# Performance work log

Hardware: AMD Instinct MI355X
Metric: run time of the kernel (lower is better)

The kernel has to match this reference:

```python
import jax, jax.numpy as jnp
import numpy as np

B = 65536
PEP, TCR, D, FF = 384, 480, 128, 512
H1, H2, OUT = 128, 64, 1
EPS = 1e-5


def _ln(x, g, b):
    mu = jnp.mean(x, axis=-1, keepdims=True)
    var = jnp.mean((x - mu) ** 2, axis=-1, keepdims=True)
    return (x - mu) * jax.lax.rsqrt(var + EPS) * g + b


def _bn(x, g, b):
    # training-mode BatchNorm1d: batch-wide stats, biased variance
    mu = jnp.mean(x, axis=0, keepdims=True)
    var = jnp.mean((x - mu) ** 2, axis=0, keepdims=True)
    return (x - mu) * jax.lax.rsqrt(var + EPS) * g + b


def setup_inputs() -> dict:
    key = jax.random.key(0)
    ks = iter(jax.random.split(key, 40))

    def w(shape, fan):
        s = float(np.sqrt(6.0 / fan))
        return jax.random.uniform(next(ks), shape, jnp.float32, -s, s)

    inp = {
        "x": jax.random.normal(next(ks), (B, PEP + TCR), jnp.float32),
        "w_pep": w((D, PEP), PEP + D), "b_pep": jnp.zeros(D),
        "w_tcr": w((D, TCR), TCR + D), "b_tcr": jnp.zeros(D),
        "wv_p2t": w((D, D), 2 * D), "bv_p2t": jnp.zeros(D),
        "wo_p2t": w((D, D), 2 * D), "bo_p2t": jnp.zeros(D),
        "wv_t2p": w((D, D), 2 * D), "bv_t2p": jnp.zeros(D),
        "wo_t2p": w((D, D), 2 * D), "bo_t2p": jnp.zeros(D),
        "ln_g1p": jnp.ones(D), "ln_b1p": jnp.zeros(D),
        "ln_g2p": jnp.ones(D), "ln_b2p": jnp.zeros(D),
        "ln_g1t": jnp.ones(D), "ln_b1t": jnp.zeros(D),
        "ln_g2t": jnp.ones(D), "ln_b2t": jnp.zeros(D),
        "ffn_w1p": w((FF, D), D + FF), "ffn_b1p": jnp.zeros(FF),
        "ffn_w2p": w((D, FF), D + FF), "ffn_b2p": jnp.zeros(D),
        "ffn_w1t": w((FF, D), D + FF), "ffn_b1t": jnp.zeros(FF),
        "ffn_w2t": w((D, FF), D + FF), "ffn_b2t": jnp.zeros(D),
        "w_h1": w((H1, 2 * D), 2 * D + H1), "b_h1": jnp.zeros(H1),
        "bn1_g": jnp.ones(H1), "bn1_b": jnp.zeros(H1),
        "w_h2": w((H2, H1), H1 + H2), "b_h2": jnp.zeros(H2),
        "bn2_g": jnp.ones(H2), "bn2_b": jnp.zeros(H2),
        "w_out": w((OUT, H2), H2 + OUT), "b_out": jnp.zeros(OUT),
    }
    return inp


def reference(x, w_pep, b_pep, w_tcr, b_tcr,
              wv_p2t, bv_p2t, wo_p2t, bo_p2t,
              wv_t2p, bv_t2p, wo_t2p, bo_t2p,
              ln_g1p, ln_b1p, ln_g2p, ln_b2p,
              ln_g1t, ln_b1t, ln_g2t, ln_b2t,
              ffn_w1p, ffn_b1p, ffn_w2p, ffn_b2p,
              ffn_w1t, ffn_b1t, ffn_w2t, ffn_b2t,
              w_h1, b_h1, bn1_g, bn1_b,
              w_h2, b_h2, bn2_g, bn2_b,
              w_out, b_out):
    pep = x[:, :PEP] @ w_pep.T + b_pep   # (B, 128)
    tcr = x[:, PEP:] @ w_tcr.T + b_tcr   # (B, 128)

    # MHA with seq_len=1: softmax over single key == 1 exactly,
    # so attention output = out_proj(v_proj(key/value input)).
    pa = (tcr @ wv_p2t.T + bv_p2t) @ wo_p2t.T + bo_p2t
    pa = _ln(pep + pa, ln_g1p, ln_b1p)
    h = jax.nn.gelu(pa @ ffn_w1p.T + ffn_b1p, approximate=False)
    pa = _ln(pa + h @ ffn_w2p.T + ffn_b2p, ln_g2p, ln_b2p)

    ta = (pep @ wv_t2p.T + bv_t2p) @ wo_t2p.T + bo_t2p
    ta = _ln(tcr + ta, ln_g1t, ln_b1t)
    h = jax.nn.gelu(ta @ ffn_w1t.T + ffn_b1t, approximate=False)
    ta = _ln(ta + h @ ffn_w2t.T + ffn_b2t, ln_g2t, ln_b2t)

    combined = jnp.concatenate([pa, ta], axis=1)  # (B, 256)
    h1 = jax.nn.gelu(_bn(combined @ w_h1.T + b_h1, bn1_g, bn1_b), approximate=False)
    h2 = jax.nn.gelu(_bn(h1 @ w_h2.T + b_h2, bn2_g, bn2_b), approximate=False)
    return h2 @ w_out.T + b_out  # (B, 1)
```

## Files before the change

kernel.cpp:

```cpp
#include <hip/hip_runtime.h>
#include <hip/hip_bf16.h>
#include <math.h>


typedef __attribute__((ext_vector_type(8))) __bf16 bf16x8;
typedef __attribute__((ext_vector_type(8))) short s16x8;
typedef __attribute__((ext_vector_type(4))) float f32x4;

union S8U { s16x8 s; bf16x8 b; };

__device__ __forceinline__ short f2b(float f) {
  return __builtin_bit_cast(short, (__bf16)f);
}
__device__ __forceinline__ float b2f(short s) {
  union { unsigned u; float f; } v; v.u = ((unsigned)(unsigned short)s) << 16;
  return v.f;
}
__device__ __forceinline__ float gelu_f(float x) {
  float u = x * __builtin_fmaf(0.035677408136f, x * x, 0.7978845608028654f);
  float e = __expf(-2.0f * u);
  return x * __builtin_amdgcn_rcpf(1.0f + e);
}

template<int NTS>
__device__ __forceinline__ void mfma_step(const short* __restrict__ Abuf, int lda, int kkA,
                                          const short* __restrict__ W, int ldw, int kw,
                                          int colbase, int l16, int q,
                                          f32x4 (&acc)[4][NTS]) {
  S8U a[4];
#pragma unroll
  for (int mt = 0; mt < 4; ++mt)
    a[mt].s = *(const s16x8*)(Abuf + (16 * mt + l16) * lda + kkA + 8 * q);
#pragma unroll
  for (int nt = 0; nt < NTS; ++nt) {
    S8U b;
    b.s = *(const s16x8*)(W + (size_t)(colbase + 16 * nt + l16) * ldw + kw + 8 * q);
#pragma unroll
    for (int mt = 0; mt < 4; ++mt)
      acc[mt][nt] = __builtin_amdgcn_mfma_f32_16x16x32_bf16(a[mt].b, b.b, acc[mt][nt], 0, 0, 0);
  }
}

template<int NTS>
__device__ __forceinline__ void zero_acc(f32x4 (&acc)[4][NTS]) {
  f32x4 z = {0.f, 0.f, 0.f, 0.f};
#pragma unroll
  for (int mt = 0; mt < 4; ++mt)
#pragma unroll
    for (int nt = 0; nt < NTS; ++nt) acc[mt][nt] = z;
}

__device__ __forceinline__ void epi_bias_store(f32x4 (&acc)[4][2], const float* __restrict__ bias,
                                               short* dst, int w, int l16, int q, bool do_gelu) {
#pragma unroll
  for (int nt = 0; nt < 2; ++nt) {
    int col = 32 * w + 16 * nt + l16;
    float bb = bias[col];
#pragma unroll
    for (int mt = 0; mt < 4; ++mt)
#pragma unroll
      for (int r = 0; r < 4; ++r) {
        int row = 16 * mt + 4 * q + r;
        float v = acc[mt][nt][r] + bb;
        if (do_gelu) v = gelu_f(v);
        dst[row * 136 + col] = f2b(v);
      }
  }
}

__device__ __forceinline__ void epi_res_ln(f32x4 (&acc)[4][2], const float* __restrict__ bias,
                                           const short* resbuf,
                                           const float* __restrict__ g, const float* __restrict__ bta,
                                           short* dst, float (*lnp)[4][2], float (*murs)[2],
                                           int w, int l16, int q, int tid) {
#pragma unroll
  for (int nt = 0; nt < 2; ++nt) {
    int col = 32 * w + 16 * nt + l16;
    float bb = bias[col];
#pragma unroll
    for (int mt = 0; mt < 4; ++mt)
#pragma unroll
      for (int r = 0; r < 4; ++r) {
        int row = 16 * mt + 4 * q + r;
        acc[mt][nt][r] += bb + b2f(resbuf[row * 136 + col]);
      }
  }
#pragma unroll
  for (int mt = 0; mt < 4; ++mt) {
#pragma unroll
    for (int r = 0; r < 4; ++r) {
      float v0 = acc[mt][0][r], v1 = acc[mt][1][r];
      float s = v0 + v1;
      float sq = v0 * v0 + v1 * v1;
#pragma unroll
      for (int off = 1; off < 16; off <<= 1) {
        s += __shfl_xor(s, off);
        sq += __shfl_xor(sq, off);
      }
      if (l16 == 0) {
        int row = 16 * mt + 4 * q + r;
        lnp[row][w][0] = s;
        lnp[row][w][1] = sq;
      }
    }
  }
  __syncthreads();
  if (tid < 64) {
    float s = lnp[tid][0][0] + lnp[tid][1][0] + lnp[tid][2][0] + lnp[tid][3][0];
    float sq = lnp[tid][0][1] + lnp[tid][1][1] + lnp[tid][2][1] + lnp[tid][3][1];
    float mu = s * (1.0f / 128.0f);
    float var = sq * (1.0f / 128.0f) - mu * mu;
    murs[tid][0] = mu;
    murs[tid][1] = rsqrtf(var + 1e-5f);
  }
  __syncthreads();
#pragma unroll
  for (int nt = 0; nt < 2; ++nt) {
    int col = 32 * w + 16 * nt + l16;
    float gg = g[col], b2 = bta[col];
#pragma unroll
    for (int mt = 0; mt < 4; ++mt)
#pragma unroll
      for (int r = 0; r < 4; ++r) {
        int row = 16 * mt + 4 * q + r;
        float v = (acc[mt][nt][r] - murs[row][0]) * murs[row][1] * gg + b2;
        dst[row * 136 + col] = f2b(v);
      }
  }
}

__device__ __forceinline__ void ffn_block(const short* __restrict__ w1, const short* __restrict__ w2,
                                          const float* __restrict__ b1, const float* __restrict__ b2,
                                          const float* __restrict__ g, const float* __restrict__ bta,
                                          short* act, short* H,
                                          float (*lnp)[4][2], float (*murs)[2],
                                          int w, int l16, int q, int tid) {
  f32x4 acc2[4][2];
  zero_acc(acc2);
  for (int c = 0; c < 4; ++c) {
    f32x4 acch[4][2];
    zero_acc(acch);
#pragma unroll
    for (int kk = 0; kk < 4; ++kk)
      mfma_step<2>(act, 136, 32 * kk, w1, 128, 32 * kk, c * 128 + 32 * w, l16, q, acch);
#pragma unroll
    for (int nt = 0; nt < 2; ++nt) {
      int lcol = 32 * w + 16 * nt + l16;
      float bb = b1[c * 128 + lcol];
#pragma unroll
      for (int mt = 0; mt < 4; ++mt)
#pragma unroll
        for (int r = 0; r < 4; ++r)
          H[(16 * mt + 4 * q + r) * 136 + lcol] = f2b(gelu_f(acch[mt][nt][r] + bb));
    }
    __syncthreads();
#pragma unroll
    for (int kk = 0; kk < 4; ++kk)
      mfma_step<2>(H, 136, 32 * kk, w2, 512, c * 128 + 32 * kk, 32 * w, l16, q, acc2);
    __syncthreads();
  }
  epi_res_ln(acc2, b2, act, g, bta, act, lnp, murs, w, l16, q, tid);
  __syncthreads();
}

struct K1Args {
  const float* x;
  const short *wpep, *wtcr, *wcp, *wct, *w1p, *w2p, *w1t, *w2t, *wh1;
  const float *bpep, *btcr, *bcp, *bct;
  const float *g1p, *e1p, *g2p, *e2p, *g1t, *e1t, *g2t, *e2t;
  const float *b1p, *b2p, *b1t, *b2t, *bh1;
  float *sum1, *sq1;
  short* h1;
};

__global__ __launch_bounds__(256, 3) void k1_main(K1Args A) {
  __shared__ __align__(16) short smem[2 * 64 * 136 + 2 * 64 * 72];
  short* U = smem;
  short* V = U + 64 * 136;
  short* Rst = V + 64 * 136;
  short* R0 = Rst;
  short* R1 = Rst + 64 * 72;
  short* Hb = Rst;
  float (*lnp)[4][2] = (float (*)[4][2])(void*)(Rst + 7936);
  float (*murs)[2] = (float (*)[2])(void*)(Rst + 8960);

  const int tid = threadIdx.x;
  const int w = tid >> 6;
  const int lane = tid & 63;
  const int l16 = lane & 15;
  const int q = lane >> 4;
  const size_t row0 = (size_t)blockIdx.x * 64;

  const int r_st = tid >> 2;
  const float* xrow = A.x + (row0 + r_st) * 864;

  float4 pf0, pf1, pf2, pf3;
  auto issue64 = [&](int kb) {
    const float* p = xrow + kb + (tid & 3) * 16;
    pf0 = *(const float4*)(p);
    pf1 = *(const float4*)(p + 4);
    pf2 = *(const float4*)(p + 8);
    pf3 = *(const float4*)(p + 12);
  };
  auto write64 = [&](short* Sb) {
    int c = (tid & 3) * 16;
    s16x8 o0, o1;
    o0[0] = f2b(pf0.x); o0[1] = f2b(pf0.y); o0[2] = f2b(pf0.z); o0[3] = f2b(pf0.w);
    o0[4] = f2b(pf1.x); o0[5] = f2b(pf1.y); o0[6] = f2b(pf1.z); o0[7] = f2b(pf1.w);
    o1[0] = f2b(pf2.x); o1[1] = f2b(pf2.y); o1[2] = f2b(pf2.z); o1[3] = f2b(pf2.w);
    o1[4] = f2b(pf3.x); o1[5] = f2b(pf3.y); o1[6] = f2b(pf3.z); o1[7] = f2b(pf3.w);
    *(s16x8*)(Sb + r_st * 72 + c) = o0;
    *(s16x8*)(Sb + r_st * 72 + c + 8) = o1;
  };
  auto issue32 = [&](int kb) {
    const float* p = xrow + kb + (tid & 3) * 8;
    pf0 = *(const float4*)(p);
    pf1 = *(const float4*)(p + 4);
  };
  auto write32 = [&](short* Sb) {
    int c = (tid & 3) * 8;
    s16x8 o0;
    o0[0] = f2b(pf0.x); o0[1] = f2b(pf0.y); o0[2] = f2b(pf0.z); o0[3] = f2b(pf0.w);
    o0[4] = f2b(pf1.x); o0[5] = f2b(pf1.y); o0[6] = f2b(pf1.z); o0[7] = f2b(pf1.w);
    *(s16x8*)(Sb + r_st * 72 + c) = o0;
  };

  f32x4 accP[4][2], accT[4][2];
  zero_acc(accP); zero_acc(accT);

  issue64(0); write64(R0);
  __syncthreads();
  for (int t = 0; t < 14; ++t) {
    short* cur = (t & 1) ? R1 : R0;
    short* nxt = (t & 1) ? R0 : R1;
    if (t < 13) { if (t == 12) issue32(832); else issue64(64 * (t + 1)); }
    if (t < 6) {
      mfma_step<2>(cur, 72, 0,  A.wpep, 384, 64 * t,      32 * w, l16, q, accP);
      mfma_step<2>(cur, 72, 32, A.wpep, 384, 64 * t + 32, 32 * w, l16, q, accP);
    } else if (t < 13) {
      mfma_step<2>(cur, 72, 0,  A.wtcr, 480, 64 * (t - 6),      32 * w, l16, q, accT);
      mfma_step<2>(cur, 72, 32, A.wtcr, 480, 64 * (t - 6) + 32, 32 * w, l16, q, accT);
    } else {
      mfma_step<2>(cur, 72, 0,  A.wtcr, 480, 448, 32 * w, l16, q, accT);
    }
    if (t < 13) { if (t == 12) write32(nxt); else write64(nxt); }
    __syncthreads();
  }
  epi_bias_store(accP, A.bpep, U, w, l16, q, false);
  epi_bias_store(accT, A.btcr, V, w, l16, q, false);
  __syncthreads();

  zero_acc(accP); zero_acc(accT);
#pragma unroll
  for (int kk = 0; kk < 4; ++kk)
    mfma_step<2>(V, 136, 32 * kk, A.wcp, 128, 32 * kk, 32 * w, l16, q, accP);
#pragma unroll
  for (int kk = 0; kk < 4; ++kk)
    mfma_step<2>(U, 136, 32 * kk, A.wct, 128, 32 * kk, 32 * w, l16, q, accT);
  epi_res_ln(accP, A.bcp, U, A.g1p, A.e1p, U, lnp, murs, w, l16, q, tid);
  epi_res_ln(accT, A.bct, V, A.g1t, A.e1t, V, lnp, murs, w, l16, q, tid);
  __syncthreads();

  ffn_block(A.w1p, A.w2p, A.b1p, A.b2p, A.g2p, A.e2p, U, Hb, lnp, murs, w, l16, q, tid);
  ffn_block(A.w1t, A.w2t, A.b1t, A.b2t, A.g2t, A.e2t, V, Hb, lnp, murs, w, l16, q, tid);

  zero_acc(accP);
#pragma unroll
  for (int s = 0; s < 8; ++s)
    mfma_step<2>((s < 4) ? U : V, 136, 32 * (s & 3), A.wh1, 256, 32 * s, 32 * w, l16, q, accP);
#pragma unroll
  for (int nt = 0; nt < 2; ++nt) {
    int col = 32 * w + 16 * nt + l16;
    float bb = A.bh1[col];
    float s = 0.f, sq = 0.f;
#pragma unroll
    for (int mt = 0; mt < 4; ++mt)
#pragma unroll
      for (int r = 0; r < 4; ++r) {
        float v = accP[mt][nt][r] + bb;
        s += v; sq += v * v;
        A.h1[(row0 + 16 * mt + 4 * q + r) * 128 + col] = f2b(v);
      }
    s += __shfl_xor(s, 16); sq += __shfl_xor(sq, 16);
    s += __shfl_xor(s, 32); sq += __shfl_xor(sq, 32);
    if (q == 0) {
      atomicAdd(&A.sum1[col], s);
      atomicAdd(&A.sq1[col], sq);
    }
  }
}

struct K2Args {
  const short* h1;
  const short* wh2;
  const float *bh2, *bn1g, *bn1b;
  const float *sum1, *sq1;
  float *sum2, *sq2;
  short* h2;
};

__global__ __launch_bounds__(256) void k2_main(K2Args A) {
  __shared__ __align__(16) short S2[64 * 136];
  __shared__ float s1[128], t1[128];
  const int tid = threadIdx.x;
  const int w = tid >> 6, lane = tid & 63, l16 = lane & 15, q = lane >> 4;
  const size_t row0 = (size_t)blockIdx.x * 64;

  if (tid < 128) {
    float su = A.sum1[tid], sq = A.sq1[tid];
    float mu = su * (1.0f / 65536.0f);
    float var = sq * (1.0f / 65536.0f) - mu * mu;
    float sc = A.bn1g[tid] * rsqrtf(var + 1e-5f);
    s1[tid] = sc;
    t1[tid] = A.bn1b[tid] - mu * sc;
  }
  __syncthreads();
  {
    int r = tid >> 2;
#pragma unroll
    for (int j = 0; j < 4; ++j) {
      int c = (tid & 3) * 32 + j * 8;
      s16x8 hv = *(const s16x8*)(A.h1 + (row0 + r) * 128 + c);
      s16x8 o;
#pragma unroll
      for (int i = 0; i < 8; ++i) {
        float f = b2f(hv[i]);
        f = gelu_f(f * s1[c + i] + t1[c + i]);
        o[i] = f2b(f);
      }
      *(s16x8*)(S2 + r * 136 + c) = o;
    }
  }
  __syncthreads();
  f32x4 acc[4][1];
  zero_acc(acc);
#pragma unroll
  for (int kk = 0; kk < 4; ++kk)
    mfma_step<1>(S2, 136, 32 * kk, A.wh2, 128, 32 * kk, 16 * w, l16, q, acc);
  int col = 16 * w + l16;
  float bb = A.bh2[col];
  float s = 0.f, sq = 0.f;
#pragma unroll
  for (int mt = 0; mt < 4; ++mt)
#pragma unroll
    for (int r = 0; r < 4; ++r) {
      float v = acc[mt][0][r] + bb;
      s += v; sq += v * v;
      A.h2[(row0 + 16 * mt + 4 * q + r) * 64 + col] = f2b(v);
    }
  s += __shfl_xor(s, 16); sq += __shfl_xor(sq, 16);
  s += __shfl_xor(s, 32); sq += __shfl_xor(sq, 32);
  if (q == 0) {
    atomicAdd(&A.sum2[col], s);
    atomicAdd(&A.sq2[col], sq);
  }
}

struct K3Args {
  const short* h2;
  const float *bn2g, *bn2b;
  const float *sum2, *sq2;
  const float *wout, *bout;
  float* out;
};

__global__ __launch_bounds__(256) void k3_main(K3Args A) {
  __shared__ float s2[64], t2[64], wo[64];
  const int tid = threadIdx.x;
  if (tid < 64) {
    float su = A.sum2[tid], sq = A.sq2[tid];
    float mu = su * (1.0f / 65536.0f);
    float var = sq * (1.0f / 65536.0f) - mu * mu;
    float sc = A.bn2g[tid] * rsqrtf(var + 1e-5f);
    s2[tid] = sc;
    t2[tid] = A.bn2b[tid] - mu * sc;
    wo[tid] = A.wout[tid];
  }
  __syncthreads();
  size_t row = (size_t)blockIdx.x * 32 + (tid >> 3);
  int c0 = (tid & 7) * 8;
  s16x8 hv = *(const s16x8*)(A.h2 + row * 64 + c0);
  float s = 0.f;
#pragma unroll
  for (int i = 0; i < 8; ++i) {
    float f = b2f(hv[i]);
    f = gelu_f(f * s2[c0 + i] + t2[c0 + i]);
    s += f * wo[c0 + i];
  }
  s += __shfl_xor(s, 1); s += __shfl_xor(s, 2); s += __shfl_xor(s, 4);
  if ((tid & 7) == 0) A.out[row] = s + A.bout[0];
}

struct CvtArgs {
  const float* src[8];
  short* dst;
  float* stats;
  const float *wv[2], *wo[2], *bv[2], *bo[2];
  short* wc[2];
  float* bc[2];
};

__global__ __launch_bounds__(256) void k0_setup(CvtArgs A) {
  int b = blockIdx.x;
  const int tid = threadIdx.x;
  if (b >= 404) {
    int b2 = b - 404, pair = b2 >> 4, part = b2 & 15;
    const float* wv = A.wv[pair];
    const float* wo = A.wo[pair];
#pragma unroll
    for (int i = 0; i < 4; ++i) {
      int idx = part * 1024 + i * 256 + tid;
      int o = idx >> 7, k = idx & 127;
      const float* worow = wo + o * 128;
      float acc = 0.f;
#pragma unroll 4
      for (int j = 0; j < 128; ++j) acc += worow[j] * wv[j * 128 + k];
      A.wc[pair][idx] = f2b(acc);
    }
    if (part == 0 && tid < 128) {
      const float* bvp = A.bv[pair];
      float acc = A.bo[pair][tid];
      for (int j = 0; j < 128; ++j) acc += wo[tid * 128 + j] * bvp[j];
      A.bc[pair][tid] = acc;
    }
    return;
  }
  const int st[8] = {0, 49152, 176128, 241664, 307200, 372736, 438272, 471040};
  if (b == 0) {
    A.stats[tid] = 0.0f;
    if (tid < 128) A.stats[256 + tid] = 0.0f;
  }
  int dstbase = b * 1024 + ((b >= 108) ? 65536 : 0);
  int seg = 0;
#pragma unroll
  for (int t = 1; t < 8; ++t) seg += (dstbase >= st[t]) ? 1 : 0;
  const float* s = A.src[seg];
  int loc = dstbase - st[seg] + tid * 4;
  float4 f = *(const float4*)(s + loc);
  int di = dstbase + tid * 4;
  A.dst[di + 0] = f2b(f.x);
  A.dst[di + 1] = f2b(f.y);
  A.dst[di + 2] = f2b(f.z);
  A.dst[di + 3] = f2b(f.w);
}

extern "C" void kernel_launch(void* const* d_in, const int* in_sizes, int n_in,
                              void* d_out, int out_size, void* d_ws, size_t ws_size,
                              hipStream_t stream) {
  (void)in_sizes; (void)n_in; (void)out_size; (void)ws_size;
  const float* x = (const float*)d_in[0];
  char* ws = (char*)d_ws;
  short* wb = (short*)ws;
  enum { O_PEP = 0, O_TCR = 49152, O_WCP = 110592, O_BCF = 126976,
         O_WCT = 143360, O_W1P = 176128, O_W2P = 241664,
         O_W1T = 307200, O_W2T = 372736, O_H1 = 438272, O_H2 = 471040 };
  float* stats = (float*)(ws + 958464);
  short* h1_pre = (short*)(ws + 960000);
  short* h2_pre = (short*)(ws + 17737216);
  float* bcomp = (float*)(ws + (size_t)O_BCF * 2);

  CvtArgs ca;
  ca.src[0] = (const float*)d_in[1];
  ca.src[1] = (const float*)d_in[3];
  ca.src[2] = (const float*)d_in[21];
  ca.src[3] = (const float*)d_in[23];
  ca.src[4] = (const float*)d_in[25];
  ca.src[5] = (const float*)d_in[27];
  ca.src[6] = (const float*)d_in[29];
  ca.src[7] = (const float*)d_in[33];
  ca.dst = wb;
  ca.stats = stats;
  ca.wv[0] = (const float*)d_in[5];   ca.bv[0] = (const float*)d_in[6];
  ca.wo[0] = (const float*)d_in[7];   ca.bo[0] = (const float*)d_in[8];
  ca.wv[1] = (const float*)d_in[9];   ca.bv[1] = (const float*)d_in[10];
  ca.wo[1] = (const float*)d_in[11];  ca.bo[1] = (const float*)d_in[12];
  ca.wc[0] = wb + O_WCP;  ca.wc[1] = wb + O_WCT;
  ca.bc[0] = bcomp;       ca.bc[1] = bcomp + 128;
  k0_setup<<<436, 256, 0, stream>>>(ca);

  K1Args a1;
  a1.x = x;
  a1.wpep = wb + O_PEP;  a1.wtcr = wb + O_TCR;
  a1.wcp = wb + O_WCP;   a1.wct = wb + O_WCT;
  a1.w1p = wb + O_W1P;   a1.w2p = wb + O_W2P;
  a1.w1t = wb + O_W1T;   a1.w2t = wb + O_W2T;
  a1.wh1 = wb + O_H1;
  a1.bpep = (const float*)d_in[2];
  a1.btcr = (const float*)d_in[4];
  a1.bcp = bcomp;
  a1.bct = bcomp + 128;
  a1.g1p = (const float*)d_in[13];  a1.e1p = (const float*)d_in[14];
  a1.g2p = (const float*)d_in[15];  a1.e2p = (const float*)d_in[16];
  a1.g1t = (const float*)d_in[17];  a1.e1t = (const float*)d_in[18];
  a1.g2t = (const float*)d_in[19];  a1.e2t = (const float*)d_in[20];
  a1.b1p = (const float*)d_in[22];
  a1.b2p = (const float*)d_in[24];
  a1.b1t = (const float*)d_in[26];
  a1.b2t = (const float*)d_in[28];
  a1.bh1 = (const float*)d_in[30];
  a1.sum1 = stats;
  a1.sq1 = stats + 128;
  a1.h1 = h1_pre;
  k1_main<<<1024, 256, 0, stream>>>(a1);

  K2Args a2;
  a2.h1 = h1_pre;
  a2.wh2 = wb + O_H2;
  a2.bh2 = (const float*)d_in[34];
  a2.bn1g = (const float*)d_in[31];
  a2.bn1b = (const float*)d_in[32];
  a2.sum1 = stats;
  a2.sq1 = stats + 128;
  a2.sum2 = stats + 256;
  a2.sq2 = stats + 320;
  a2.h2 = h2_pre;
  k2_main<<<1024, 256, 0, stream>>>(a2);

  K3Args a3;
  a3.h2 = h2_pre;
  a3.bn2g = (const float*)d_in[35];
  a3.bn2b = (const float*)d_in[36];
  a3.sum2 = stats + 256;
  a3.sq2 = stats + 320;
  a3.wout = (const float*)d_in[37];
  a3.bout = (const float*)d_in[38];
  a3.out = (float*)d_out;
  k3_main<<<2048, 256, 0, stream>>>(a3);
}
```

Before: 568.8 us.

## Software-pipeline FFN hidden chunks and deepen x prefetch to two stages

The FFN block now processes 64-wide hidden chunks through double-buffered H tiles in the R0/R1 scratch. The next chunk's first GEMM and GELU store overlap the second GEMM on the current chunk, so one barrier per chunk replaces two. The input staging loop now keeps two register prefetch sets, loading two tiles ahead to hide global latency, at the cost of more registers. The setup kernel also stages wv in 64KB of shared memory for the fused weight product, which raises LDS use in that small kernel.

Measured after the change: 553.7 us. -2.7%, faster.

```diff
diff --git a/kernel.cpp b/kernel.cpp
--- a/kernel.cpp
+++ b/kernel.cpp
@@ -129,34 +129,49 @@
   }
 }
 
+__device__ __forceinline__ void store_h(short* H, f32x4 (&a)[4][1], const float* __restrict__ b1c,
+                                        int w, int l16, int q) {
+  int lcol = 16 * w + l16;
+  float bb = b1c[lcol];
+#pragma unroll
+  for (int mt = 0; mt < 4; ++mt)
+#pragma unroll
+    for (int r = 0; r < 4; ++r)
+      H[(16 * mt + 4 * q + r) * 72 + lcol] = f2b(gelu_f(a[mt][0][r] + bb));
+}
+
 __device__ __forceinline__ void ffn_block(const short* __restrict__ w1, const short* __restrict__ w2,
                                           const float* __restrict__ b1, const float* __restrict__ b2,
                                           const float* __restrict__ g, const float* __restrict__ bta,
-                                          short* act, short* H,
+                                          short* act, short* H0, short* H1,
                                           float (*lnp)[4][2], float (*murs)[2],
                                           int w, int l16, int q, int tid) {
   f32x4 acc2[4][2];
   zero_acc(acc2);
-  for (int c = 0; c < 4; ++c) {
-    f32x4 acch[4][2];
+  {
+    f32x4 acch[4][1];
     zero_acc(acch);
 #pragma unroll
     for (int kk = 0; kk < 4; ++kk)
-      mfma_step<2>(act, 136, 32 * kk, w1, 128, 32 * kk, c * 128 + 32 * w, l16, q, acch);
-#pragma unroll
-    for (int nt = 0; nt < 2; ++nt) {
-      int lcol = 32 * w + 16 * nt + l16;
-      float bb = b1[c * 128 + lcol];
-#pragma unroll
-      for (int mt = 0; mt < 4; ++mt)
-#pragma unroll
-        for (int r = 0; r < 4; ++r)
-          H[(16 * mt + 4 * q + r) * 136 + lcol] = f2b(gelu_f(acch[mt][nt][r] + bb));
-    }
-    __syncthreads();
-#pragma unroll
-    for (int kk = 0; kk < 4; ++kk)
-      mfma_step<2>(H, 136, 32 * kk, w2, 512, c * 128 + 32 * kk, 32 * w, l16, q, acc2);
+      mfma_step<1>(act, 136, 32 * kk, w1, 128, 32 * kk, 16 * w, l16, q, acch);
+    store_h(H0, acch, b1, w, l16, q);
+  }
+  __syncthreads();
+#pragma unroll
+  for (int c = 0; c < 8; ++c) {
+    short* Hr = (c & 1) ? H1 : H0;
+    short* Hw = (c & 1) ? H0 : H1;
+    f32x4 accn[4][1];
+    if (c < 7) {
+      zero_acc(accn);
+#pragma unroll
+      for (int kk = 0; kk < 4; ++kk)
+        mfma_step<1>(act, 136, 32 * kk, w1, 128, 32 * kk, (c + 1) * 64 + 16 * w, l16, q, accn);
+    }
+#pragma unroll
+    for (int kk = 0; kk < 2; ++kk)
+      mfma_step<2>(Hr, 72, 32 * kk, w2, 512, c * 64 + 32 * kk, 32 * w, l16, q, acc2);
+    if (c < 7) store_h(Hw, accn, b1 + (c + 1) * 64, w, l16, q);
     __syncthreads();
   }
   epi_res_ln(acc2, b2, act, g, bta, act, lnp, murs, w, l16, q, tid);
@@ -180,7 +195,6 @@
   short* Rst = V + 64 * 136;
   short* R0 = Rst;
   short* R1 = Rst + 64 * 72;
-  short* Hb = Rst;
   float (*lnp)[4][2] = (float (*)[4][2])(void*)(Rst + 7936);
   float (*murs)[2] = (float (*)[2])(void*)(Rst + 8960);
 
@@ -194,46 +208,53 @@
   const int r_st = tid >> 2;
   const float* xrow = A.x + (row0 + r_st) * 864;
 
-  float4 pf0, pf1, pf2, pf3;
-  auto issue64 = [&](int kb) {
+  float4 pA[4], pB[4];
+  auto ld64 = [&](int kb, float4 (&pf)[4]) {
     const float* p = xrow + kb + (tid & 3) * 16;
-    pf0 = *(const float4*)(p);
-    pf1 = *(const float4*)(p + 4);
-    pf2 = *(const float4*)(p + 8);
-    pf3 = *(const float4*)(p + 12);
+    pf[0] = *(const float4*)(p);
+    pf[1] = *(const float4*)(p + 4);
+    pf[2] = *(const float4*)(p + 8);
+    pf[3] = *(const float4*)(p + 12);
   };
-  auto write64 = [&](short* Sb) {
+  auto ld32 = [&](int kb, float4 (&pf)[4]) {
+    const float* p = xrow + kb + (tid & 3) * 8;
+    pf[0] = *(const float4*)(p);
+    pf[1] = *(const float4*)(p + 4);
+  };
+  auto st64 = [&](short* Sb, float4 (&pf)[4]) {
     int c = (tid & 3) * 16;
     s16x8 o0, o1;
-    o0[0] = f2b(pf0.x); o0[1] = f2b(pf0.y); o0[2] = f2b(pf0.z); o0[3] = f2b(pf0.w);
-    o0[4] = f2b(pf1.x); o0[5] = f2b(pf1.y); o0[6] = f2b(pf1.z); o0[7] = f2b(pf1.w);
-    o1[0] = f2b(pf2.x); o1[1] = f2b(pf2.y); o1[2] = f2b(pf2.z); o1[3] = f2b(pf2.w);
-    o1[4] = f2b(pf3.x); o1[5] = f2b(pf3.y); o1[6] = f2b(pf3.z); o1[7] = f2b(pf3.w);
+    o0[0] = f2b(pf[0].x); o0[1] = f2b(pf[0].y); o0[2] = f2b(pf[0].z); o0[3] = f2b(pf[0].w);
+    o0[4] = f2b(pf[1].x); o0[5] = f2b(pf[1].y); o0[6] = f2b(pf[1].z); o0[7] = f2b(pf[1].w);
+    o1[0] = f2b(pf[2].x); o1[1] = f2b(pf[2].y); o1[2] = f2b(pf[2].z); o1[3] = f2b(pf[2].w);
+    o1[4] = f2b(pf[3].x); o1[5] = f2b(pf[3].y); o1[6] = f2b(pf[3].z); o1[7] = f2b(pf[3].w);
     *(s16x8*)(Sb + r_st * 72 + c) = o0;
     *(s16x8*)(Sb + r_st * 72 + c + 8) = o1;
   };
-  auto issue32 = [&](int kb) {
-    const float* p = xrow + kb + (tid & 3) * 8;
-    pf0 = *(const float4*)(p);
-    pf1 = *(const float4*)(p + 4);
-  };
-  auto write32 = [&](short* Sb) {
+  auto st32 = [&](short* Sb, float4 (&pf)[4]) {
     int c = (tid & 3) * 8;
     s16x8 o0;
-    o0[0] = f2b(pf0.x); o0[1] = f2b(pf0.y); o0[2] = f2b(pf0.z); o0[3] = f2b(pf0.w);
-    o0[4] = f2b(pf1.x); o0[5] = f2b(pf1.y); o0[6] = f2b(pf1.z); o0[7] = f2b(pf1.w);
+    o0[0] = f2b(pf[0].x); o0[1] = f2b(pf[0].y); o0[2] = f2b(pf[0].z); o0[3] = f2b(pf[0].w);
+    o0[4] = f2b(pf[1].x); o0[5] = f2b(pf[1].y); o0[6] = f2b(pf[1].z); o0[7] = f2b(pf[1].w);
     *(s16x8*)(Sb + r_st * 72 + c) = o0;
   };
 
   f32x4 accP[4][2], accT[4][2];
   zero_acc(accP); zero_acc(accT);
 
-  issue64(0); write64(R0);
-  __syncthreads();
+  ld64(0, pA);
+  ld64(64, pB);
+  st64(R0, pA);
+  __syncthreads();
+#pragma unroll
   for (int t = 0; t < 14; ++t) {
+    if (t + 2 < 13) {
+      if (t & 1) ld64(64 * (t + 2), pB); else ld64(64 * (t + 2), pA);
+    } else if (t + 2 == 13) {
+      if (t & 1) ld32(832, pB); else ld32(832, pA);
+    }
     short* cur = (t & 1) ? R1 : R0;
     short* nxt = (t & 1) ? R0 : R1;
-    if (t < 13) { if (t == 12) issue32(832); else issue64(64 * (t + 1)); }
     if (t < 6) {
       mfma_step<2>(cur, 72, 0,  A.wpep, 384, 64 * t,      32 * w, l16, q, accP);
       mfma_step<2>(cur, 72, 32, A.wpep, 384, 64 * t + 32, 32 * w, l16, q, accP);
@@ -243,7 +264,11 @@
     } else {
       mfma_step<2>(cur, 72, 0,  A.wtcr, 480, 448, 32 * w, l16, q, accT);
     }
-    if (t < 13) { if (t == 12) write32(nxt); else write64(nxt); }
+    if (t + 1 < 13) {
+      if (t & 1) st64(nxt, pA); else st64(nxt, pB);
+    } else if (t + 1 == 13) {
+      if (t & 1) st32(nxt, pA); else st32(nxt, pB);
+    }
     __syncthreads();
   }
   epi_bias_store(accP, A.bpep, U, w, l16, q, false);
@@ -261,8 +286,8 @@
   epi_res_ln(accT, A.bct, V, A.g1t, A.e1t, V, lnp, murs, w, l16, q, tid);
   __syncthreads();
 
-  ffn_block(A.w1p, A.w2p, A.b1p, A.b2p, A.g2p, A.e2p, U, Hb, lnp, murs, w, l16, q, tid);
-  ffn_block(A.w1t, A.w2t, A.b1t, A.b2t, A.g2t, A.e2t, V, Hb, lnp, murs, w, l16, q, tid);
+  ffn_block(A.w1p, A.w2p, A.b1p, A.b2p, A.g2p, A.e2p, U, R0, R1, lnp, murs, w, l16, q, tid);
+  ffn_block(A.w1t, A.w2t, A.b1t, A.b2t, A.g2t, A.e2t, V, R0, R1, lnp, murs, w, l16, q, tid);
 
   zero_acc(accP);
 #pragma unroll
@@ -401,6 +426,7 @@
 };
 
 __global__ __launch_bounds__(256) void k0_setup(CvtArgs A) {
+  __shared__ float wvs[128 * 128];
   int b = blockIdx.x;
   const int tid = threadIdx.x;
   if (b >= 404) {
@@ -408,13 +434,19 @@
     const float* wv = A.wv[pair];
     const float* wo = A.wo[pair];
 #pragma unroll
+    for (int i = 0; i < 16; ++i) {
+      int idx4 = (i * 256 + tid) * 4;
+      *(float4*)(wvs + idx4) = *(const float4*)(wv + idx4);
+    }
+    __syncthreads();
+#pragma unroll
     for (int i = 0; i < 4; ++i) {
       int idx = part * 1024 + i * 256 + tid;
       int o = idx >> 7, k = idx & 127;
       const float* worow = wo + o * 128;
       float acc = 0.f;
 #pragma unroll 4
-      for (int j = 0; j < 128; ++j) acc += worow[j] * wv[j * 128 + k];
+      for (int j = 0; j < 128; ++j) acc += worow[j] * wvs[j * 128 + k];
       A.wc[pair][idx] = f2b(acc);
     }
     if (part == 0 && tid < 128) {
```
